# Optimization experiments

Hardware: AMD Instinct MI355X
Metric: run time of the kernel (lower is better)

Reference implementation:

```python
import jax, jax.numpy as jnp
import numpy as np

B, C, N, K, OUT = 4, 192, 10000, 16, 384

def setup_inputs() -> dict:
    key = jax.random.key(0)
    k1, k2, k3, k4 = jax.random.split(key, 4)
    x = jax.random.normal(k1, (B, C, N, 1), dtype=jnp.float32)
    edge_index = jax.random.randint(k2, (2, B, N, K), 0, N, dtype=jnp.int32)
    # 1x1x1 Conv3d weight [OUT, 2C, 1, 1, 1] collapsed to [OUT, 2C]
    fan_in = 2 * C
    weight = jax.random.normal(k3, (OUT, 2 * C), dtype=jnp.float32) / np.sqrt(fan_in)
    bias = jax.random.normal(k4, (OUT,), dtype=jnp.float32) * 0.01
    return {"x": x, "edge_index": edge_index, "weight": weight, "bias": bias}


def _gather_neighbors(x3, idx):
    # x3: [B, C, N], idx: [B, N, K] -> [B, C, N, K]
    return jax.vmap(lambda xb, ib: xb[:, ib])(x3, idx)


def reference(x, edge_index, weight, bias):
    b, c, n, _ = x.shape
    x3 = x[..., 0]                                   # [B, C, N]
    x_i = _gather_neighbors(x3, edge_index[1])       # centers  [B, C, N, K]
    x_j = _gather_neighbors(x3, edge_index[0])       # neighbors [B, C, N, K]
    x_j_max = jnp.max(x_j - x_i, axis=-1)            # max-relative, [B, C, N]
    # torch.cat([x.unsqueeze(2), x_j.unsqueeze(2)], 2).reshape(b, 2c, n, 1)
    # interleaves channels as (x_c, xj_c) pairs
    feat = jnp.stack([x3, x_j_max], axis=2).reshape(b, 2 * c, n)  # [B, 2C, N]
    out = jnp.einsum('oc,bcn->bon', weight, feat) + bias[None, :, None]
    out = jax.nn.relu(out)
    # Conv3d path: output shape [B, OUT, N, 1, 1]
    return out[..., None, None]
```

## Files before the change

### kernel.cpp

```cpp
#include <hip/hip_runtime.h>
#include <hip/hip_bf16.h>


#define NB   4
#define NC   192
#define NN   10000
#define NK   16
#define NOUT 384
#define K2C  384

typedef short bf16x8 __attribute__((ext_vector_type(8)));
typedef float f32x4  __attribute__((ext_vector_type(4)));

__device__ inline unsigned short f2bf(float f) {
    unsigned int u = __builtin_bit_cast(unsigned int, f);
    u += ((u >> 16) & 1u) + 0x7FFFu;
    return (unsigned short)(u >> 16);
}
__device__ inline float bflo(unsigned int u) { return __builtin_bit_cast(float, u << 16); }
__device__ inline float bfhi(unsigned int u) { return __builtin_bit_cast(float, u & 0xFFFF0000u); }

__global__ __launch_bounds__(256) void k_prep(const float* __restrict__ x,
                                              const float* __restrict__ w,
                                              unsigned short* __restrict__ xT,
                                              unsigned short* __restrict__ wbf) {
    __shared__ unsigned short tile[NC * 65];
    int gid = blockIdx.x * 256 + threadIdx.x;
    if (gid < NOUT * K2C) wbf[gid] = f2bf(w[gid]);

    int b  = blockIdx.x & 3;
    int nb = (blockIdx.x >> 2) * 64;
    int t  = threadIdx.x;
    const float* xb = x + (size_t)b * NC * NN;
    for (int i = 0; i < 48; ++i) {
        int idx = i * 256 + t;
        int c  = idx >> 6;
        int nl = idx & 63;
        int n  = nb + nl;
        float v = (n < NN) ? xb[(size_t)c * NN + n] : 0.f;
        tile[c * 65 + nl] = f2bf(v);
    }
    __syncthreads();
    unsigned int* xTd = (unsigned int*)(xT + (size_t)b * NN * NC);
    for (int i = 0; i < 24; ++i) {
        int idx = i * 256 + t;
        int nl  = idx / 96;
        int cd  = idx - nl * 96;
        int n   = nb + nl;
        if (n < NN) {
            unsigned int lo = tile[(2 * cd)     * 65 + nl];
            unsigned int hi = tile[(2 * cd + 1) * 65 + nl];
            xTd[(size_t)n * 96 + cd] = lo | (hi << 16);
        }
    }
}

__global__ __launch_bounds__(256, 3) void k_fused(const unsigned short* __restrict__ wbf,
                                                  const unsigned short* __restrict__ xT,
                                                  const int* __restrict__ eidx,
                                                  const float* __restrict__ bias,
                                                  float* __restrict__ out) {
    __shared__ unsigned short lds[64 * 48 * 8];
    int bid  = blockIdx.x;
    int b    = bid & 3;
    int nt   = bid >> 2;
    int wv   = threadIdx.x >> 6;
    int lane = threadIdx.x & 63;

    const uint4* xr4 = (const uint4*)(xT + (size_t)b * NN * NC);
    const int* e0 = eidx + (size_t)b * NN * NK;
    const int* e1 = eidx + (size_t)NB * NN * NK + (size_t)b * NN * NK;
    int nbase = nt * 64 + wv * 16;

    int vj[4], vi[4];
#pragma unroll
    for (int i = 0; i < 4; ++i) {
        int idx = i * 64 + lane;
        int n   = nbase + (idx >> 4);
        vj[i] = (n < NN) ? e0[(size_t)nbase * NK + idx] : 0;
        vi[i] = (n < NN) ? e1[(size_t)nbase * NK + idx] : 0;
    }
    int d = lane;
    bool act = (d < 24);

#pragma unroll
    for (int qq = 0; qq < 4; ++qq) {
        int vjq = vj[qq], viq = vi[qq];
        for (int it2 = 0; it2 < 4; ++it2) {
            int it = qq * 4 + it2;
            int n  = nbase + it;
            if (n < NN) {
                int nl = wv * 16 + it;
                uint4 cx = make_uint4(0, 0, 0, 0);
                if (act) cx = xr4[(size_t)n * 24 + d];
                float m[8];
#pragma unroll
                for (int c = 0; c < 8; ++c) m[c] = -1e30f;
#pragma unroll
                for (int k = 0; k < 16; ++k) {
                    int sl  = it2 * 16 + k;
                    int jn  = __shfl(vjq, sl, 64);
                    int in_ = __shfl(viq, sl, 64);
                    uint4 jr = make_uint4(0, 0, 0, 0), ir = make_uint4(0, 0, 0, 0);
                    if (act) { jr = xr4[(size_t)jn * 24 + d]; ir = xr4[(size_t)in_ * 24 + d]; }
                    m[0] = fmaxf(m[0], bflo(jr.x) - bflo(ir.x));
                    m[1] = fmaxf(m[1], bfhi(jr.x) - bfhi(ir.x));
                    m[2] = fmaxf(m[2], bflo(jr.y) - bflo(ir.y));
                    m[3] = fmaxf(m[3], bfhi(jr.y) - bfhi(ir.y));
                    m[4] = fmaxf(m[4], bflo(jr.z) - bflo(ir.z));
                    m[5] = fmaxf(m[5], bfhi(jr.z) - bfhi(ir.z));
                    m[6] = fmaxf(m[6], bflo(jr.w) - bflo(ir.w));
                    m[7] = fmaxf(m[7], bfhi(jr.w) - bfhi(ir.w));
                }
                if (act) {
                    unsigned int mm[4];
#pragma unroll
                    for (int c = 0; c < 4; ++c)
                        mm[c] = (unsigned int)f2bf(m[2 * c]) | ((unsigned int)f2bf(m[2 * c + 1]) << 16);
                    uint4 g0, g1;
                    g0.x = (cx.x & 0xFFFFu) | (mm[0] << 16);
                    g0.y = (cx.x >> 16)     | (mm[0] & 0xFFFF0000u);
                    g0.z = (cx.y & 0xFFFFu) | (mm[1] << 16);
                    g0.w = (cx.y >> 16)     | (mm[1] & 0xFFFF0000u);
                    g1.x = (cx.z & 0xFFFFu) | (mm[2] << 16);
                    g1.y = (cx.z >> 16)     | (mm[2] & 0xFFFF0000u);
                    g1.z = (cx.w & 0xFFFFu) | (mm[3] << 16);
                    g1.w = (cx.w >> 16)     | (mm[3] & 0xFFFF0000u);
                    int s0 = nl * 48 + (2 * d     + 3 * nl) % 48;
                    int s1 = nl * 48 + (2 * d + 1 + 3 * nl) % 48;
                    *(uint4*)&lds[(size_t)s0 * 8] = g0;
                    *(uint4*)&lds[(size_t)s1 * 8] = g1;
                }
            }
        }
    }

    int r = lane & 15;
    int q = lane >> 4;
    const unsigned short* aptr = wbf + (size_t)(wv * 96 + r) * K2C + q * 8;
    unsigned int nbs[4], u0[4];
#pragma unroll
    for (int ni = 0; ni < 4; ++ni) {
        unsigned int n_ = ni * 16 + r;
        nbs[ni] = n_ * 48u;
        u0[ni]  = ((unsigned int)q + 3u * n_) % 48u;
    }
    f32x4 acc[6][4];
#pragma unroll
    for (int mi = 0; mi < 6; ++mi)
#pragma unroll
        for (int ni = 0; ni < 4; ++ni)
            acc[mi][ni] = (f32x4){0.f, 0.f, 0.f, 0.f};

    __syncthreads();

#pragma unroll 2
    for (int t = 0; t < 12; ++t) {
        bf16x8 a[6], bb[4];
#pragma unroll
        for (int mi = 0; mi < 6; ++mi)
            a[mi] = *(const bf16x8*)(aptr + (size_t)mi * 16 * K2C + t * 32);
#pragma unroll
        for (int ni = 0; ni < 4; ++ni) {
            unsigned int u = u0[ni] + 4u * t;
            if (u >= 48u) u -= 48u;
            bb[ni] = *(const bf16x8*)(lds + (size_t)(nbs[ni] + u) * 8);
        }
#pragma unroll
        for (int mi = 0; mi < 6; ++mi)
#pragma unroll
            for (int ni = 0; ni < 4; ++ni)
                acc[mi][ni] = __builtin_amdgcn_mfma_f32_16x16x32_bf16(a[mi], bb[ni], acc[mi][ni], 0, 0, 0);
    }

    float* ob = out + (size_t)b * NOUT * NN;
#pragma unroll
    for (int mi = 0; mi < 6; ++mi) {
        int obase = wv * 96 + mi * 16 + q * 4;
        float4 b4 = *(const float4*)(bias + obase);
#pragma unroll
        for (int ni = 0; ni < 4; ++ni) {
            int n = nt * 64 + ni * 16 + r;
            if (n < NN) {
                float bv[4] = {b4.x, b4.y, b4.z, b4.w};
#pragma unroll
                for (int rr = 0; rr < 4; ++rr) {
                    float val = acc[mi][ni][rr] + bv[rr];
                    ob[(size_t)(obase + rr) * NN + n] = fmaxf(val, 0.f);
                }
            }
        }
    }
}

extern "C" void kernel_launch(void* const* d_in, const int* in_sizes, int n_in,
                              void* d_out, int out_size, void* d_ws, size_t ws_size,
                              hipStream_t stream) {
    const float* x    = (const float*)d_in[0];
    const int*   eidx = (const int*)d_in[1];
    const float* w    = (const float*)d_in[2];
    const float* bias = (const float*)d_in[3];
    float* out = (float*)d_out;

    unsigned short* xT  = (unsigned short*)d_ws;
    unsigned short* wbf = xT + (size_t)NB * NN * NC;

    hipLaunchKernelGGL(k_prep,  dim3(4 * 157), dim3(256), 0, stream, x, w, xT, wbf);
    hipLaunchKernelGGL(k_fused, dim3(4 * 157), dim3(256), 0, stream, wbf, xT, eidx, bias, out);
}
```

Measured before the change: 196.4 us.

## Switch to fp16 packed max-relative gather with smaller node tiles and fp16 MFMA

```diff
diff --git a/kernel.cpp b/kernel.cpp
--- a/kernel.cpp
+++ b/kernel.cpp
@@ -1,5 +1,4 @@
 #include <hip/hip_runtime.h>
-#include <hip/hip_bf16.h>
 
 
 #define NB   4
@@ -9,24 +8,22 @@
 #define NOUT 384
 #define K2C  384
 
-typedef short bf16x8 __attribute__((ext_vector_type(8)));
-typedef float f32x4  __attribute__((ext_vector_type(4)));
+typedef _Float16 f16x8 __attribute__((ext_vector_type(8)));
+typedef _Float16 h2    __attribute__((ext_vector_type(2)));
+typedef float    f32x4 __attribute__((ext_vector_type(4)));
 
-__device__ inline unsigned short f2bf(float f) {
-    unsigned int u = __builtin_bit_cast(unsigned int, f);
-    u += ((u >> 16) & 1u) + 0x7FFFu;
-    return (unsigned short)(u >> 16);
+__device__ inline unsigned short f2h(float f) {
+    _Float16 h = (_Float16)f;
+    return __builtin_bit_cast(unsigned short, h);
 }
-__device__ inline float bflo(unsigned int u) { return __builtin_bit_cast(float, u << 16); }
-__device__ inline float bfhi(unsigned int u) { return __builtin_bit_cast(float, u & 0xFFFF0000u); }
 
 __global__ __launch_bounds__(256) void k_prep(const float* __restrict__ x,
                                               const float* __restrict__ w,
                                               unsigned short* __restrict__ xT,
-                                              unsigned short* __restrict__ wbf) {
+                                              unsigned short* __restrict__ wh) {
     __shared__ unsigned short tile[NC * 65];
     int gid = blockIdx.x * 256 + threadIdx.x;
-    if (gid < NOUT * K2C) wbf[gid] = f2bf(w[gid]);
+    if (gid < NOUT * K2C) wh[gid] = f2h(w[gid]);
 
     int b  = blockIdx.x & 3;
     int nb = (blockIdx.x >> 2) * 64;
@@ -38,7 +35,7 @@
         int nl = idx & 63;
         int n  = nb + nl;
         float v = (n < NN) ? xb[(size_t)c * NN + n] : 0.f;
-        tile[c * 65 + nl] = f2bf(v);
+        tile[c * 65 + nl] = f2h(v);
     }
     __syncthreads();
     unsigned int* xTd = (unsigned int*)(xT + (size_t)b * NN * NC);
@@ -55,122 +52,91 @@
     }
 }
 
-__global__ __launch_bounds__(256, 3) void k_fused(const unsigned short* __restrict__ wbf,
+__global__ __launch_bounds__(256, 4) void k_fused(const unsigned short* __restrict__ wh,
                                                   const unsigned short* __restrict__ xT,
                                                   const int* __restrict__ eidx,
                                                   const float* __restrict__ bias,
                                                   float* __restrict__ out) {
-    __shared__ unsigned short lds[64 * 48 * 8];
+    __shared__ unsigned short lds[32 * 49 * 8];
     int bid  = blockIdx.x;
     int b    = bid & 3;
     int nt   = bid >> 2;
     int wv   = threadIdx.x >> 6;
     int lane = threadIdx.x & 63;
 
-    const uint4* xr4 = (const uint4*)(xT + (size_t)b * NN * NC);
+    const uint2* xr2 = (const uint2*)(xT + (size_t)b * NN * NC);
     const int* e0 = eidx + (size_t)b * NN * NK;
     const int* e1 = eidx + (size_t)NB * NN * NK + (size_t)b * NN * NK;
-    int nbase = nt * 64 + wv * 16;
+    int nbase = nt * 32 + wv * 8;
 
-    int vj[4], vi[4];
+    int ej[2], ei[2];
 #pragma unroll
-    for (int i = 0; i < 4; ++i) {
+    for (int i = 0; i < 2; ++i) {
         int idx = i * 64 + lane;
-        int n   = nbase + (idx >> 4);
-        vj[i] = (n < NN) ? e0[(size_t)nbase * NK + idx] : 0;
-        vi[i] = (n < NN) ? e1[(size_t)nbase * NK + idx] : 0;
+        int nn  = nbase + (idx >> 4);
+        ej[i] = (nn < NN) ? e0[(size_t)nbase * NK + idx] : 0;
+        ei[i] = (nn < NN) ? e1[(size_t)nbase * NK + idx] : 0;
     }
-    int d = lane;
-    bool act = (d < 24);
+    int dc = (lane < 48) ? lane : 47;
 
+#pragma unroll 1
+    for (int it = 0; it < 8; ++it) {
+        int n = nbase + it;
+        if (n < NN) {
+            int nl = wv * 8 + it;
+            uint2 cx = xr2[(size_t)n * 48 + dc];
+            h2 m0 = __builtin_bit_cast(h2, 0xFC00FC00u);
+            h2 m1 = m0;
 #pragma unroll
-    for (int qq = 0; qq < 4; ++qq) {
-        int vjq = vj[qq], viq = vi[qq];
-        for (int it2 = 0; it2 < 4; ++it2) {
-            int it = qq * 4 + it2;
-            int n  = nbase + it;
-            if (n < NN) {
-                int nl = wv * 16 + it;
-                uint4 cx = make_uint4(0, 0, 0, 0);
-                if (act) cx = xr4[(size_t)n * 24 + d];
-                float m[8];
-#pragma unroll
-                for (int c = 0; c < 8; ++c) m[c] = -1e30f;
-#pragma unroll
-                for (int k = 0; k < 16; ++k) {
-                    int sl  = it2 * 16 + k;
-                    int jn  = __shfl(vjq, sl, 64);
-                    int in_ = __shfl(viq, sl, 64);
-                    uint4 jr = make_uint4(0, 0, 0, 0), ir = make_uint4(0, 0, 0, 0);
-                    if (act) { jr = xr4[(size_t)jn * 24 + d]; ir = xr4[(size_t)in_ * 24 + d]; }
-                    m[0] = fmaxf(m[0], bflo(jr.x) - bflo(ir.x));
-                    m[1] = fmaxf(m[1], bfhi(jr.x) - bfhi(ir.x));
-                    m[2] = fmaxf(m[2], bflo(jr.y) - bflo(ir.y));
-                    m[3] = fmaxf(m[3], bfhi(jr.y) - bfhi(ir.y));
-                    m[4] = fmaxf(m[4], bflo(jr.z) - bflo(ir.z));
-                    m[5] = fmaxf(m[5], bfhi(jr.z) - bfhi(ir.z));
-                    m[6] = fmaxf(m[6], bflo(jr.w) - bflo(ir.w));
-                    m[7] = fmaxf(m[7], bfhi(jr.w) - bfhi(ir.w));
-                }
-                if (act) {
-                    unsigned int mm[4];
-#pragma unroll
-                    for (int c = 0; c < 4; ++c)
-                        mm[c] = (unsigned int)f2bf(m[2 * c]) | ((unsigned int)f2bf(m[2 * c + 1]) << 16);
-                    uint4 g0, g1;
-                    g0.x = (cx.x & 0xFFFFu) | (mm[0] << 16);
-                    g0.y = (cx.x >> 16)     | (mm[0] & 0xFFFF0000u);
-                    g0.z = (cx.y & 0xFFFFu) | (mm[1] << 16);
-                    g0.w = (cx.y >> 16)     | (mm[1] & 0xFFFF0000u);
-                    g1.x = (cx.z & 0xFFFFu) | (mm[2] << 16);
-                    g1.y = (cx.z >> 16)     | (mm[2] & 0xFFFF0000u);
-                    g1.z = (cx.w & 0xFFFFu) | (mm[3] << 16);
-                    g1.w = (cx.w >> 16)     | (mm[3] & 0xFFFF0000u);
-                    int s0 = nl * 48 + (2 * d     + 3 * nl) % 48;
-                    int s1 = nl * 48 + (2 * d + 1 + 3 * nl) % 48;
-                    *(uint4*)&lds[(size_t)s0 * 8] = g0;
-                    *(uint4*)&lds[(size_t)s1 * 8] = g1;
-                }
+            for (int k = 0; k < 16; ++k) {
+                int j  = __builtin_amdgcn_readlane(ej[it >> 2], ((it & 3) * 16) + k);
+                int i_ = __builtin_amdgcn_readlane(ei[it >> 2], ((it & 3) * 16) + k);
+                uint2 jr = xr2[(size_t)j  * 48 + dc];
+                uint2 ir = xr2[(size_t)i_ * 48 + dc];
+                h2 dlo = __builtin_bit_cast(h2, jr.x) - __builtin_bit_cast(h2, ir.x);
+                h2 dhi = __builtin_bit_cast(h2, jr.y) - __builtin_bit_cast(h2, ir.y);
+                m0 = __builtin_elementwise_max(m0, dlo);
+                m1 = __builtin_elementwise_max(m1, dhi);
             }
+            unsigned int mb0 = __builtin_bit_cast(unsigned int, m0);
+            unsigned int mb1 = __builtin_bit_cast(unsigned int, m1);
+            uint4 g;
+            g.x = (cx.x & 0xFFFFu) | (mb0 << 16);
+            g.y = (cx.x >> 16)     | (mb0 & 0xFFFF0000u);
+            g.z = (cx.y & 0xFFFFu) | (mb1 << 16);
+            g.w = (cx.y >> 16)     | (mb1 & 0xFFFF0000u);
+            *(uint4*)&lds[(size_t)(nl * 49 + dc) * 8] = g;
         }
     }
 
     int r = lane & 15;
     int q = lane >> 4;
-    const unsigned short* aptr = wbf + (size_t)(wv * 96 + r) * K2C + q * 8;
-    unsigned int nbs[4], u0[4];
-#pragma unroll
-    for (int ni = 0; ni < 4; ++ni) {
-        unsigned int n_ = ni * 16 + r;
-        nbs[ni] = n_ * 48u;
-        u0[ni]  = ((unsigned int)q + 3u * n_) % 48u;
-    }
-    f32x4 acc[6][4];
+    const unsigned short* aptr = wh + (size_t)(wv * 96 + r) * K2C + q * 8;
+    f32x4 acc[6][2];
 #pragma unroll
     for (int mi = 0; mi < 6; ++mi)
 #pragma unroll
-        for (int ni = 0; ni < 4; ++ni)
+        for (int ni = 0; ni < 2; ++ni)
             acc[mi][ni] = (f32x4){0.f, 0.f, 0.f, 0.f};
 
     __syncthreads();
 
 #pragma unroll 2
     for (int t = 0; t < 12; ++t) {
-        bf16x8 a[6], bb[4];
+        f16x8 a[6], bb[2];
 #pragma unroll
         for (int mi = 0; mi < 6; ++mi)
-            a[mi] = *(const bf16x8*)(aptr + (size_t)mi * 16 * K2C + t * 32);
+            a[mi] = *(const f16x8*)(aptr + (size_t)mi * 16 * K2C + t * 32);
 #pragma unroll
-        for (int ni = 0; ni < 4; ++ni) {
-            unsigned int u = u0[ni] + 4u * t;
-            if (u >= 48u) u -= 48u;
-            bb[ni] = *(const bf16x8*)(lds + (size_t)(nbs[ni] + u) * 8);
+        for (int ni = 0; ni < 2; ++ni) {
+            int row = ni * 16 + r;
+            bb[ni] = *(const f16x8*)&lds[(size_t)(row * 49 + 4 * t + q) * 8];
         }
 #pragma unroll
         for (int mi = 0; mi < 6; ++mi)
 #pragma unroll
-            for (int ni = 0; ni < 4; ++ni)
-                acc[mi][ni] = __builtin_amdgcn_mfma_f32_16x16x32_bf16(a[mi], bb[ni], acc[mi][ni], 0, 0, 0);
+            for (int ni = 0; ni < 2; ++ni)
+                acc[mi][ni] = __builtin_amdgcn_mfma_f32_16x16x32_f16(a[mi], bb[ni], acc[mi][ni], 0, 0, 0);
     }
 
     float* ob = out + (size_t)b * NOUT * NN;
@@ -178,11 +144,11 @@
     for (int mi = 0; mi < 6; ++mi) {
         int obase = wv * 96 + mi * 16 + q * 4;
         float4 b4 = *(const float4*)(bias + obase);
+        float bv[4] = {b4.x, b4.y, b4.z, b4.w};
 #pragma unroll
-        for (int ni = 0; ni < 4; ++ni) {
-            int n = nt * 64 + ni * 16 + r;
+        for (int ni = 0; ni < 2; ++ni) {
+            int n = nt * 32 + ni * 16 + r;
             if (n < NN) {
-                float bv[4] = {b4.x, b4.y, b4.z, b4.w};
 #pragma unroll
                 for (int rr = 0; rr < 4; ++rr) {
                     float val = acc[mi][ni][rr] + bv[rr];
@@ -202,9 +168,9 @@
     const float* bias = (const float*)d_in[3];
     float* out = (float*)d_out;
 
-    unsigned short* xT  = (unsigned short*)d_ws;
-    unsigned short* wbf = xT + (size_t)NB * NN * NC;
+    unsigned short* xT = (unsigned short*)d_ws;
+    unsigned short* wh = xT + (size_t)NB * NN * NC;
 
-    hipLaunchKernelGGL(k_prep,  dim3(4 * 157), dim3(256), 0, stream, x, w, xT, wbf);
-    hipLaunchKernelGGL(k_fused, dim3(4 * 157), dim3(256), 0, stream, wbf, xT, eidx, bias, out);
+    hipLaunchKernelGGL(k_prep,  dim3(4 * 157), dim3(256), 0, stream, x, w, xT, wh);
+    hipLaunchKernelGGL(k_fused, dim3(4 * 313), dim3(256), 0, stream, wh, xT, eidx, bias, out);
 }
```

After: 195.2 us. No clear change (-0.6%).
